# Kernel tuning notes

Hardware: AMD Instinct MI355X
Metric: run time of the kernel (lower is better)

## Reference

```python
import jax, jax.numpy as jnp
import numpy as np
import math

D_MODEL = 2048
N_HEADS = 16
D_K = D_MODEL // N_HEADS
B = 4
S = 2048


def setup_inputs() -> dict:
    key = jax.random.key(0)
    ks = jax.random.split(key, 12)
    sd = 1.0 / math.sqrt(D_MODEL)
    inp = {
        "query": jax.random.normal(ks[0], (B, S, D_MODEL), dtype=jnp.float32),
        "key": jax.random.normal(ks[1], (B, S, D_MODEL), dtype=jnp.float32),
        "value": jax.random.normal(ks[2], (B, S, D_MODEL), dtype=jnp.float32),
        # causal mask: 1 where attendable, 0 where masked (mask == 0 -> -1e9)
        "mask": jnp.tril(jnp.ones((1, 1, S, S), dtype=jnp.int32)),
        "W_q": jax.random.uniform(ks[3], (D_MODEL, D_MODEL), jnp.float32, -sd, sd),
        "b_q": jnp.zeros((D_MODEL,), jnp.float32),
        "W_k": jax.random.uniform(ks[4], (D_MODEL, D_MODEL), jnp.float32, -sd, sd),
        "b_k": jnp.zeros((D_MODEL,), jnp.float32),
        "W_v": jax.random.uniform(ks[5], (D_MODEL, D_MODEL), jnp.float32, -sd, sd),
        "b_v": jnp.zeros((D_MODEL,), jnp.float32),
        "W_o": jax.random.uniform(ks[6], (D_MODEL, D_MODEL), jnp.float32, -sd, sd),
        "b_o": jnp.zeros((D_MODEL,), jnp.float32),
    }
    return inp


def reference(query, key, value, mask, W_q, b_q, W_k, b_k, W_v, b_v, W_o, b_o):
    scale = math.sqrt(D_K)
    # QKV projections + split heads: [B, S, D] -> [B, H, S, d_k]
    def split_heads(x):
        return x.reshape(B, -1, N_HEADS, D_K).transpose(0, 2, 1, 3)

    Q = split_heads(query @ W_q.T + b_q)
    K = split_heads(key @ W_k.T + b_k)
    V = split_heads(value @ W_v.T + b_v)

    # scores: [B, H, Sq, Sk]
    scores = jnp.einsum("bhqd,bhkd->bhqk", Q, K) / scale
    scores = jnp.where(mask == 0, jnp.float32(-1e9), scores)
    attn = jax.nn.softmax(scores, axis=-1)
    # context: [B, H, Sq, d_k] -> [B, Sq, D]
    ctx = jnp.einsum("bhqk,bhkd->bhqd", attn, V)
    ctx = ctx.transpose(0, 2, 1, 3).reshape(B, S, D_MODEL)
    return ctx @ W_o.T + b_o
```

## Files before the change

kernel.cpp:

```cpp
#include <hip/hip_runtime.h>
#include <stdint.h>

#define D_MODEL 2048
#define S_LEN 2048
#define BATCH 4
#define NHEADS 16
#define DK 128
#define M_TOK (BATCH * S_LEN)

typedef __attribute__((ext_vector_type(8))) short bf16x8;
typedef __attribute__((ext_vector_type(4))) float f32x4;

__device__ __forceinline__ short f2bf(float f) {
  unsigned u = __float_as_uint(f);
  u = (u + 0x7FFF + ((u >> 16) & 1)) >> 16;
  return (short)u;
}

__device__ __forceinline__ void gl2lds16(const void* g, void* l) {
  __builtin_amdgcn_global_load_lds(
      (const __attribute__((address_space(1))) unsigned int*)g,
      (__attribute__((address_space(3))) unsigned int*)l, 16, 0, 0);
}

#define ASM_BAR() asm volatile("s_barrier" ::: "memory")
#define VMCNT0() asm volatile("s_waitcnt vmcnt(0)" ::: "memory")

__global__ __launch_bounds__(256) void cvt_kernel(const float* __restrict__ in,
                                                  short* __restrict__ out,
                                                  int n8) {
  int i = blockIdx.x * blockDim.x + threadIdx.x;
  const int stride = gridDim.x * blockDim.x;
  for (; i < n8; i += stride) {
    const float4* p = (const float4*)(in + (size_t)i * 8);
    float4 a = p[0], b = p[1];
    bf16x8 o;
    o[0] = f2bf(a.x); o[1] = f2bf(a.y); o[2] = f2bf(a.z); o[3] = f2bf(a.w);
    o[4] = f2bf(b.x); o[5] = f2bf(b.y); o[6] = f2bf(b.z); o[7] = f2bf(b.w);
    *(bf16x8*)(out + (size_t)i * 8) = o;
  }
}

template <int EPI>
__global__ __launch_bounds__(512, 2) void gemm256(const short* __restrict__ A,
                                                  const short* __restrict__ B,
                                                  const float* __restrict__ bias,
                                                  void* __restrict__ Cout) {
  __shared__ short As[2][256 * 64];
  __shared__ short Bs[2][256 * 64];
  const int t = threadIdx.x, lane = t & 63, w = t >> 6;
  const int c = lane & 15, g = lane >> 4;
  const int wr = w >> 2, wc = w & 3;

  const int cpx = (int)gridDim.x >> 3;
  const int swz = ((int)blockIdx.x & 7) * cpx + ((int)blockIdx.x >> 3);
  const int by = swz >> 3, bx = swz & 7;
  const int row0 = by * 256, col0 = bx * 256;
  const int K = D_MODEL;
  const int NT = K / 64;

  const int srow = t >> 3;
  const int sseg = t & 7;
  const int skk = 8 * (sseg ^ (srow & 7));

  const short* Abase = A + (size_t)(row0 + srow) * K;
  const short* Bbase = B + (size_t)(col0 + srow) * K;

#define SWEEPA(p, R, kt)                                              \
  gl2lds16(Abase + (size_t)(R) * 64 * K + (kt) * 64 + skk,            \
           &As[p][(R) * 4096 + t * 8])
#define SWEEPB(p, R, kt)                                              \
  gl2lds16(Bbase + (size_t)(R) * 64 * K + (kt) * 64 + skk,            \
           &Bs[p][(R) * 4096 + t * 8])
#define STAGE_TILE(q, kt1)                                            \
  {                                                                   \
    SWEEPA(q, 0, kt1); SWEEPA(q, 1, kt1);                             \
    SWEEPA(q, 2, kt1); SWEEPA(q, 3, kt1);                             \
    SWEEPB(q, 0, kt1); SWEEPB(q, 1, kt1);                             \
    SWEEPB(q, 2, kt1); SWEEPB(q, 3, kt1);                             \
  }

  f32x4 acc[8][4] = {};

  STAGE_TILE(0, 0);

  for (int kt = 0; kt < NT; ++kt) {
    const int p = kt & 1, q = p ^ 1;
    VMCNT0();
    ASM_BAR();
    if (kt + 1 < NT) STAGE_TILE(q, kt + 1);

    const char* abase = (const char*)As[p];
    const char* bbase = (const char*)Bs[p];
#pragma unroll
    for (int ks = 0; ks < 2; ++ks) {
      const int kb = (ks * 64 + g * 16) ^ ((c & 7) << 4);
      bf16x8 bfr[4];
#pragma unroll
      for (int ni = 0; ni < 4; ++ni)
        bfr[ni] = *(const bf16x8*)(bbase + (wc * 64 + ni * 16 + c) * 128 + kb);
#pragma unroll
      for (int mg = 0; mg < 2; ++mg) {
        bf16x8 afr[4];
#pragma unroll
        for (int mi = 0; mi < 4; ++mi)
          afr[mi] = *(const bf16x8*)(abase +
                                     (wr * 128 + mg * 64 + mi * 16 + c) * 128 +
                                     kb);
        __builtin_amdgcn_s_setprio(1);
#pragma unroll
        for (int mi = 0; mi < 4; ++mi)
#pragma unroll
          for (int ni = 0; ni < 4; ++ni)
            acc[mg * 4 + mi][ni] = __builtin_amdgcn_mfma_f32_16x16x32_bf16(
                afr[mi], bfr[ni], acc[mg * 4 + mi][ni], 0, 0, 0);
        __builtin_amdgcn_s_setprio(0);
      }
    }
  }

#pragma unroll
  for (int ni = 0; ni < 4; ++ni) {
    const int col = col0 + wc * 64 + ni * 16 + c;
    const float bv = bias[col];
#pragma unroll
    for (int m = 0; m < 8; ++m) {
      const int rbase = row0 + wr * 128 + (m >> 2) * 64 + (m & 3) * 16 + g * 4;
      if (EPI == 2) {
        const int h = col >> 7, dk = col & 127;
        const int b = rbase >> 11, s0 = rbase & 2047;
        ushort4 pk;
        pk.x = (unsigned short)f2bf(acc[m][ni][0] + bv);
        pk.y = (unsigned short)f2bf(acc[m][ni][1] + bv);
        pk.z = (unsigned short)f2bf(acc[m][ni][2] + bv);
        pk.w = (unsigned short)f2bf(acc[m][ni][3] + bv);
        *(ushort4*)&((short*)Cout)[(((size_t)b * NHEADS + h) * DK + dk) *
                                       S_LEN + s0] = pk;
      } else {
#pragma unroll
        for (int r = 0; r < 4; ++r) {
          const int row = rbase + r;
          const float v = acc[m][ni][r] + bv;
          if (EPI == 0) {
            const int b = row >> 11, s = row & 2047;
            const int h = col >> 7, dk = col & 127;
            ((short*)Cout)[(((size_t)b * NHEADS + h) * S_LEN + s) * DK + dk] =
                f2bf(v);
          } else {
            ((float*)Cout)[(size_t)row * D_MODEL + col] = v;
          }
        }
      }
    }
  }
#undef SWEEPA
#undef SWEEPB
#undef STAGE_TILE
}

__global__ __launch_bounds__(256, 2) void attn_kernel(
    const short* __restrict__ Qp, const short* __restrict__ Kp,
    const short* __restrict__ Vt, short* __restrict__ ctx) {
  const int t = threadIdx.x, lane = t & 63, w = t >> 6;
  const int c = lane & 15, g = lane >> 4;

  const int fid = blockIdx.x;
  const int x = fid & 7, u = fid >> 3;
  const int bh = ((u & 7) << 3) | x;
  const int qt = 15 - (u >> 3);
  const int b = bh >> 4, h = bh & 15;

  __shared__ short Kl[2][64 * 128];
  __shared__ short Vl[2][128 * 64];
  __shared__ short Pl[4][32][64];

  const short* Kbase = Kp + (size_t)bh * S_LEN * DK;
  const short* Vbase = Vt + (size_t)bh * DK * S_LEN;

  const int qbase = qt * 128 + w * 32;
  const short* Qg = Qp + ((size_t)bh * S_LEN + qbase + c) * DK;
  bf16x8 aq[2][4];
#pragma unroll
  for (int mi = 0; mi < 2; ++mi)
#pragma unroll
    for (int kc = 0; kc < 4; ++kc)
      aq[mi][kc] = *(const bf16x8*)(Qg + mi * 16 * DK + kc * 32 + g * 8);

  float mprev[2][4], lsum[2][4];
  f32x4 accO[2][8] = {};
#pragma unroll
  for (int mi = 0; mi < 2; ++mi)
#pragma unroll
    for (int r = 0; r < 4; ++r) {
      mprev[mi][r] = -3.0e38f;
      lsum[mi][r] = 0.f;
    }
  const float cexp = 0.12753101829629947f;

  const int nt = 2 * qt + 2;
  const int jmax = (qbase + 31) >> 6;

  auto stage = [&](int buf, int j) {
    const short* Kg = Kbase + (size_t)j * 64 * DK;
#pragma unroll
    for (int ii = 0; ii < 4; ++ii) {
      int s = t + 256 * ii;
      int row = s >> 4, cs = s & 15;
      gl2lds16(Kg + row * DK + (cs ^ (row & 7)) * 8, &Kl[buf][s * 8]);
    }
    const short* Vg = Vbase + j * 64;
#pragma unroll
    for (int ii = 0; ii < 4; ++ii) {
      int s = t + 256 * ii;
      int row = s >> 3, cs = s & 7;
      gl2lds16(Vg + (size_t)row * S_LEN + (cs ^ (row & 7)) * 8,
               &Vl[buf][s * 8]);
    }
  };

  stage(0, 0);
  __syncthreads();
  int cur = 0;

  for (int j = 0; j < nt; ++j) {
    if (j + 1 < nt) stage(cur ^ 1, j + 1);

    if (j <= jmax) {
      f32x4 sa[2][4];
#pragma unroll
      for (int mi = 0; mi < 2; ++mi)
#pragma unroll
        for (int nf = 0; nf < 4; ++nf) sa[mi][nf] = (f32x4){0.f, 0.f, 0.f, 0.f};
      __builtin_amdgcn_s_setprio(1);
#pragma unroll
      for (int nf = 0; nf < 4; ++nf) {
#pragma unroll
        for (int kc = 0; kc < 4; ++kc) {
          const int row = nf * 16 + c;
          const int seg = kc * 4 + g;
          bf16x8 bk = *(const bf16x8*)((const char*)&Kl[cur][0] + row * 256 +
                                       ((seg ^ (row & 7)) << 4));
#pragma unroll
          for (int mi = 0; mi < 2; ++mi)
            sa[mi][nf] = __builtin_amdgcn_mfma_f32_16x16x32_bf16(
                aq[mi][kc], bk, sa[mi][nf], 0, 0, 0);
        }
      }
      __builtin_amdgcn_s_setprio(0);

#pragma unroll
      for (int mi = 0; mi < 2; ++mi) {
        if (j * 64 + 63 > qbase + mi * 16) {
#pragma unroll
          for (int r = 0; r < 4; ++r) {
            const int qglob = qbase + mi * 16 + g * 4 + r;
#pragma unroll
            for (int nf = 0; nf < 4; ++nf)
              if ((j * 64 + nf * 16 + c) > qglob) sa[mi][nf][r] = -3.0e38f;
          }
        }
      }

      float mt[2][4];
      bool need = false;
#pragma unroll
      for (int mi = 0; mi < 2; ++mi)
#pragma unroll
        for (int r = 0; r < 4; ++r) {
          float m0 = fmaxf(fmaxf(sa[mi][0][r], sa[mi][1][r]),
                           fmaxf(sa[mi][2][r], sa[mi][3][r]));
          m0 = fmaxf(m0, __shfl_xor(m0, 1));
          m0 = fmaxf(m0, __shfl_xor(m0, 2));
          m0 = fmaxf(m0, __shfl_xor(m0, 4));
          m0 = fmaxf(m0, __shfl_xor(m0, 8));
          mt[mi][r] = m0;
          need = need || (m0 > mprev[mi][r] + 40.f);
        }
      const bool full = __any((int)need);

#pragma unroll
      for (int mi = 0; mi < 2; ++mi)
#pragma unroll
        for (int r = 0; r < 4; ++r) {
          float nm = mprev[mi][r];
          if (full) {
            nm = fmaxf(nm, mt[mi][r]);
            const float corr = exp2f((mprev[mi][r] - nm) * cexp);
            lsum[mi][r] *= corr;
#pragma unroll
            for (int no = 0; no < 8; ++no) accO[mi][no][r] *= corr;
            mprev[mi][r] = nm;
          }
          const int prow = mi * 16 + g * 4 + r;
          float rs = 0.f;
#pragma unroll
          for (int nf = 0; nf < 4; ++nf) {
            const float pp = exp2f((sa[mi][nf][r] - nm) * cexp);
            rs += pp;
            const int col = nf * 16 + c;
            *(short*)((char*)&Pl[w][0][0] + prow * 128 +
                      (((col >> 3) ^ (prow & 7)) << 4) + (col & 7) * 2) =
                f2bf(pp);
          }
          rs += __shfl_xor(rs, 1);
          rs += __shfl_xor(rs, 2);
          rs += __shfl_xor(rs, 4);
          rs += __shfl_xor(rs, 8);
          lsum[mi][r] += rs;
        }

      bf16x8 ap[2][2];
#pragma unroll
      for (int mi = 0; mi < 2; ++mi)
#pragma unroll
        for (int kc = 0; kc < 2; ++kc) {
          const int prow = mi * 16 + c;
          const int kseg = kc * 4 + g;
          ap[mi][kc] = *(const bf16x8*)((const char*)&Pl[w][0][0] +
                                        prow * 128 +
                                        ((kseg ^ (prow & 7)) << 4));
        }
      __builtin_amdgcn_s_setprio(1);
#pragma unroll
      for (int no = 0; no < 8; ++no) {
#pragma unroll
        for (int kc = 0; kc < 2; ++kc) {
          const int row = no * 16 + c;
          const int seg = kc * 4 + g;
          bf16x8 bv = *(const bf16x8*)((const char*)&Vl[cur][0] + row * 128 +
                                       ((seg ^ (row & 7)) << 4));
#pragma unroll
          for (int mi = 0; mi < 2; ++mi)
            accO[mi][no] = __builtin_amdgcn_mfma_f32_16x16x32_bf16(
                ap[mi][kc], bv, accO[mi][no], 0, 0, 0);
        }
      }
      __builtin_amdgcn_s_setprio(0);
    }

    __syncthreads();
    cur ^= 1;
  }

#pragma unroll
  for (int mi = 0; mi < 2; ++mi) {
    const int qrow = qbase + mi * 16 + g * 4;
#pragma unroll
    for (int r = 0; r < 4; ++r) {
      const float inv = 1.f / lsum[mi][r];
#pragma unroll
      for (int no = 0; no < 8; ++no) {
        ctx[((size_t)b * S_LEN + qrow + r) * D_MODEL + h * DK + no * 16 + c] =
            f2bf(accO[mi][no][r] * inv);
      }
    }
  }
}

extern "C" void kernel_launch(void* const* d_in, const int* in_sizes, int n_in,
                              void* d_out, int out_size, void* d_ws,
                              size_t ws_size, hipStream_t stream) {
  const float* query = (const float*)d_in[0];
  const float* key = (const float*)d_in[1];
  const float* value = (const float*)d_in[2];
  const float* W_q = (const float*)d_in[4];
  const float* b_q = (const float*)d_in[5];
  const float* W_k = (const float*)d_in[6];
  const float* b_k = (const float*)d_in[7];
  const float* W_v = (const float*)d_in[8];
  const float* b_v = (const float*)d_in[9];
  const float* W_o = (const float*)d_in[10];
  const float* b_o = (const float*)d_in[11];
  float* out = (float*)d_out;

  char* p = (char*)d_ws;
  const size_t WSZ = (size_t)D_MODEL * D_MODEL * 2;
  const size_t XSZ = (size_t)M_TOK * D_MODEL * 2;
  short* wq = (short*)p; p += WSZ;
  short* wk = (short*)p; p += WSZ;
  short* wv = (short*)p; p += WSZ;
  short* wo = (short*)p; p += WSZ;
  short* xq = (short*)p; p += XSZ;
  short* xk = (short*)p; p += XSZ;
  short* xv = (short*)p; p += XSZ;
  short* Qp = (short*)p; p += XSZ;
  short* Kp = (short*)p; p += XSZ;

  const int nX8 = (M_TOK * D_MODEL) / 8;
  const int nW8 = (D_MODEL * D_MODEL) / 8;
  cvt_kernel<<<2048, 256, 0, stream>>>(query, xq, nX8);
  cvt_kernel<<<2048, 256, 0, stream>>>(key, xk, nX8);
  cvt_kernel<<<2048, 256, 0, stream>>>(value, xv, nX8);
  cvt_kernel<<<2048, 256, 0, stream>>>(W_q, wq, nW8);
  cvt_kernel<<<2048, 256, 0, stream>>>(W_k, wk, nW8);
  cvt_kernel<<<2048, 256, 0, stream>>>(W_v, wv, nW8);
  cvt_kernel<<<2048, 256, 0, stream>>>(W_o, wo, nW8);

  const int ngemm = (M_TOK / 256) * (D_MODEL / 256);
  gemm256<0><<<ngemm, 512, 0, stream>>>(xq, wq, b_q, Qp);
  gemm256<0><<<ngemm, 512, 0, stream>>>(xk, wk, b_k, Kp);
  gemm256<2><<<ngemm, 512, 0, stream>>>(xv, wv, b_v, xk);

  attn_kernel<<<dim3(16 * BATCH * NHEADS), 256, 0, stream>>>(Qp, Kp, xk, xq);

  gemm256<1><<<ngemm, 512, 0, stream>>>(xq, wo, b_o, out);
}
```

Baseline: 533.5 us.

## Phase GEMM inner loop with barriers; defer softmax max/sum reductions in attention

The GEMM inner loop is split into explicit phases, each loading A fragments and issuing MFMAs between workgroup barriers with sched_barrier, so waves interleave LDS reads and matrix work in lockstep. In attention, the cross-lane max reduction now runs only when the lazy-rescale threshold triggers, and each lane keeps a partial row sum that is reduced once at the end. This removes shuffle work from the per-tile softmax hot path. The trade-offs are extra barriers in the GEMM, and the lazy-rescale check now uses lane-local maxima.

New measurement: 547.3 us. 2.6% more time.

```diff
diff --git a/kernel.cpp b/kernel.cpp
--- a/kernel.cpp
+++ b/kernel.cpp
@@ -81,6 +81,33 @@
   }
 
   f32x4 acc[8][4] = {};
+  bf16x8 bfr[4];
+
+#define LD_B(KS)                                                          \
+  {                                                                       \
+    const int kb = ((KS) * 64 + g * 16) ^ ((c & 7) << 4);                 \
+    _Pragma("unroll") for (int ni = 0; ni < 4; ++ni) bfr[ni] =            \
+        *(const bf16x8*)(bbase + (wc * 64 + ni * 16 + c) * 128 + kb);     \
+  }
+#define PHASE(KS, MG)                                                     \
+  {                                                                       \
+    const int kb = ((KS) * 64 + g * 16) ^ ((c & 7) << 4);                 \
+    bf16x8 afr[4];                                                        \
+    _Pragma("unroll") for (int mi = 0; mi < 4; ++mi) afr[mi] =            \
+        *(const bf16x8*)(abase + (wr * 128 + (MG) * 64 + mi * 16 + c) *   \
+                                     128 + kb);                           \
+    ASM_BAR();                                                            \
+    __builtin_amdgcn_s_setprio(1);                                        \
+    _Pragma("unroll") for (int mi = 0; mi < 4; ++mi) {                    \
+      _Pragma("unroll") for (int ni = 0; ni < 4; ++ni) {                  \
+        acc[(MG) * 4 + mi][ni] = __builtin_amdgcn_mfma_f32_16x16x32_bf16( \
+            afr[mi], bfr[ni], acc[(MG) * 4 + mi][ni], 0, 0, 0);           \
+      }                                                                   \
+    }                                                                     \
+    __builtin_amdgcn_s_setprio(0);                                        \
+    __builtin_amdgcn_sched_barrier(0);                                    \
+    ASM_BAR();                                                            \
+  }
 
   STAGE_TILE(0, 0);
 
@@ -88,35 +115,15 @@
     const int p = kt & 1, q = p ^ 1;
     VMCNT0();
     ASM_BAR();
-    if (kt + 1 < NT) STAGE_TILE(q, kt + 1);
-
     const char* abase = (const char*)As[p];
     const char* bbase = (const char*)Bs[p];
-#pragma unroll
-    for (int ks = 0; ks < 2; ++ks) {
-      const int kb = (ks * 64 + g * 16) ^ ((c & 7) << 4);
-      bf16x8 bfr[4];
-#pragma unroll
-      for (int ni = 0; ni < 4; ++ni)
-        bfr[ni] = *(const bf16x8*)(bbase + (wc * 64 + ni * 16 + c) * 128 + kb);
-#pragma unroll
-      for (int mg = 0; mg < 2; ++mg) {
-        bf16x8 afr[4];
-#pragma unroll
-        for (int mi = 0; mi < 4; ++mi)
-          afr[mi] = *(const bf16x8*)(abase +
-                                     (wr * 128 + mg * 64 + mi * 16 + c) * 128 +
-                                     kb);
-        __builtin_amdgcn_s_setprio(1);
-#pragma unroll
-        for (int mi = 0; mi < 4; ++mi)
-#pragma unroll
-          for (int ni = 0; ni < 4; ++ni)
-            acc[mg * 4 + mi][ni] = __builtin_amdgcn_mfma_f32_16x16x32_bf16(
-                afr[mi], bfr[ni], acc[mg * 4 + mi][ni], 0, 0, 0);
-        __builtin_amdgcn_s_setprio(0);
-      }
-    }
+    if (kt + 1 < NT) STAGE_TILE(q, kt + 1);
+    LD_B(0);
+    PHASE(0, 0);
+    PHASE(0, 1);
+    LD_B(1);
+    PHASE(1, 0);
+    PHASE(1, 1);
   }
 
 #pragma unroll
@@ -156,6 +163,8 @@
 #undef SWEEPA
 #undef SWEEPB
 #undef STAGE_TILE
+#undef LD_B
+#undef PHASE
 }
 
 __global__ __launch_bounds__(256, 2) void attn_kernel(
@@ -261,36 +270,41 @@
         }
       }
 
-      float mt[2][4];
+      float lmax[2][4];
       bool need = false;
 #pragma unroll
       for (int mi = 0; mi < 2; ++mi)
 #pragma unroll
         for (int r = 0; r < 4; ++r) {
-          float m0 = fmaxf(fmaxf(sa[mi][0][r], sa[mi][1][r]),
-                           fmaxf(sa[mi][2][r], sa[mi][3][r]));
-          m0 = fmaxf(m0, __shfl_xor(m0, 1));
-          m0 = fmaxf(m0, __shfl_xor(m0, 2));
-          m0 = fmaxf(m0, __shfl_xor(m0, 4));
-          m0 = fmaxf(m0, __shfl_xor(m0, 8));
-          mt[mi][r] = m0;
+          const float m0 = fmaxf(fmaxf(sa[mi][0][r], sa[mi][1][r]),
+                                 fmaxf(sa[mi][2][r], sa[mi][3][r]));
+          lmax[mi][r] = m0;
           need = need || (m0 > mprev[mi][r] + 40.f);
         }
-      const bool full = __any((int)need);
-
-#pragma unroll
-      for (int mi = 0; mi < 2; ++mi)
-#pragma unroll
-        for (int r = 0; r < 4; ++r) {
-          float nm = mprev[mi][r];
-          if (full) {
-            nm = fmaxf(nm, mt[mi][r]);
+      if (__any((int)need)) {
+#pragma unroll
+        for (int mi = 0; mi < 2; ++mi)
+#pragma unroll
+          for (int r = 0; r < 4; ++r) {
+            float m0 = lmax[mi][r];
+            m0 = fmaxf(m0, __shfl_xor(m0, 1));
+            m0 = fmaxf(m0, __shfl_xor(m0, 2));
+            m0 = fmaxf(m0, __shfl_xor(m0, 4));
+            m0 = fmaxf(m0, __shfl_xor(m0, 8));
+            const float nm = fmaxf(mprev[mi][r], m0);
             const float corr = exp2f((mprev[mi][r] - nm) * cexp);
             lsum[mi][r] *= corr;
 #pragma unroll
             for (int no = 0; no < 8; ++no) accO[mi][no][r] *= corr;
             mprev[mi][r] = nm;
           }
+      }
+
+#pragma unroll
+      for (int mi = 0; mi < 2; ++mi)
+#pragma unroll
+        for (int r = 0; r < 4; ++r) {
+          const float nm = mprev[mi][r];
           const int prow = mi * 16 + g * 4 + r;
           float rs = 0.f;
 #pragma unroll
@@ -302,10 +316,6 @@
                       (((col >> 3) ^ (prow & 7)) << 4) + (col & 7) * 2) =
                 f2bf(pp);
           }
-          rs += __shfl_xor(rs, 1);
-          rs += __shfl_xor(rs, 2);
-          rs += __shfl_xor(rs, 4);
-          rs += __shfl_xor(rs, 8);
           lsum[mi][r] += rs;
         }
 
@@ -347,7 +357,12 @@
     const int qrow = qbase + mi * 16 + g * 4;
 #pragma unroll
     for (int r = 0; r < 4; ++r) {
-      const float inv = 1.f / lsum[mi][r];
+      float ls = lsum[mi][r];
+      ls += __shfl_xor(ls, 1);
+      ls += __shfl_xor(ls, 2);
+      ls += __shfl_xor(ls, 4);
+      ls += __shfl_xor(ls, 8);
+      const float inv = 1.f / ls;
 #pragma unroll
       for (int no = 0; no < 8; ++no) {
         ctx[((size_t)b * S_LEN + qrow + r) * D_MODEL + h * DK + no * 16 + c] =
```
